# Kernel optimization log

Measured on AMD Instinct MI355X. Metric: run time of the kernel, lower is better.

The kernel has to match this reference:

```python
import jax, jax.numpy as jnp
import numpy as np

N = 20000        # total nodes in batched graph
E = 160000       # edges (avg in-degree 8)
D_IN = 512
D_OUT = 512
MAX_DEG = 10
BN_EPS = 1e-5


def setup_inputs() -> dict:
    key = jax.random.key(0)
    ks = jax.random.split(key, 8)
    feats = jax.random.normal(ks[0], (N, D_IN), dtype=jnp.float32)
    src = jax.random.randint(ks[1], (E,), 0, N)
    dst = jax.random.randint(ks[2], (E,), 0, N)
    # Wl[d], bl[d]: lins_l for degree d (d>=1); Wl[0] is never used since h==0 for deg-0 nodes.
    # Wr[0], bl[0] play the role of lin_zero_deg; Wr[d] (d>=1) are the bias-free lins_r.
    Wl = jax.random.normal(ks[3], (MAX_DEG + 1, D_IN, D_OUT), dtype=jnp.float32) * 0.02
    Wr = jax.random.normal(ks[4], (MAX_DEG + 1, D_IN, D_OUT), dtype=jnp.float32) * 0.02
    bl = jax.random.normal(ks[5], (MAX_DEG + 1, D_OUT), dtype=jnp.float32) * 0.02
    gamma = jnp.ones((D_OUT,), dtype=jnp.float32)
    beta = jnp.zeros((D_OUT,), dtype=jnp.float32)
    return {"feats": feats, "src": src, "dst": dst, "Wl": Wl, "Wr": Wr,
            "bl": bl, "gamma": gamma, "beta": beta}


def reference(feats, src, dst, Wl, Wr, bl, gamma, beta):
    # 1) neighbor sum: h[v] = sum_{(u->v) in E} feats[u]   (fn.copy_u + fn.sum)
    h = jax.ops.segment_sum(feats[src], dst, num_segments=N)  # [N, D_IN]
    # in-degrees, clamped to max_degree
    deg = jnp.clip(jax.ops.segment_sum(jnp.ones((E,), dtype=jnp.int32), dst,
                                       num_segments=N), 0, MAX_DEG)  # [N]
    # 2) degree-bucketed linears, vectorized over the 11 buckets then gathered per node.
    #    out[n] = h[n] @ Wl[deg[n]] + feats[n] @ Wr[deg[n]] + bl[deg[n]]
    #    deg==0 nodes have h==0, so this reduces to lin_zero_deg(feats) = feats@Wr[0]+bl[0].
    Hl = jnp.einsum('ni,dio->dno', h, Wl)      # [11, N, D_OUT]
    Hr = jnp.einsum('ni,dio->dno', feats, Wr)  # [11, N, D_OUT]
    out = (Hl + Hr + bl[:, None, :])[deg, jnp.arange(N)]  # [N, D_OUT]
    # 3) batchnorm (training mode: batch stats, biased variance)
    mean = out.mean(axis=0)
    var = out.var(axis=0)
    out = (out - mean) * jax.lax.rsqrt(var + BN_EPS) * gamma + beta
    # 4) max aggregation over graph with self loops (fn.copy_u + fn.max)
    self_ids = jnp.arange(N)
    src_s = jnp.concatenate([src, self_ids])
    dst_s = jnp.concatenate([dst, self_ids])
    out = jax.ops.segment_max(out[src_s], dst_s, num_segments=N)  # [N, D_OUT]
    return out
```

## Files before the change

kernel.cpp:

```cpp
#include <hip/hip_runtime.h>
#include <hip/hip_bf16.h>
#include <stdint.h>

#define N_NODES 20000
#define N_EDGES 160000
#define DIN 512
#define DOUT 512
#define NBUCKET 11
#define KDIM 1024
#define MAXTILES 90
#define BN_EPS 1e-5f
#define CAP 64
#define CAST_BLOCKS (N_NODES / 4)
#define WT_BLOCKS ((KDIM / 32) * (DOUT / 32) * NBUCKET)
#define BUCKET_BLOCKS ((N_NODES + 255) / 256)

typedef float f32x4 __attribute__((ext_vector_type(4)));
typedef __attribute__((ext_vector_type(8))) __bf16 bf16x8;

static __device__ __forceinline__ unsigned short f2bf(float f) {
    union { float f; unsigned u; } v; v.f = f;
    unsigned r = v.u + 0x7FFFu + ((v.u >> 16) & 1u);
    return (unsigned short)(r >> 16);
}
static __device__ __forceinline__ float bflo(unsigned p) {
    union { unsigned u; float f; } v; v.u = p << 16; return v.f;
}
static __device__ __forceinline__ float bfhi(unsigned p) {
    union { unsigned u; float f; } v; v.u = p & 0xFFFF0000u; return v.f;
}
static __device__ __forceinline__ unsigned packbf(float lo, float hi) {
    return (unsigned)f2bf(lo) | ((unsigned)f2bf(hi) << 16);
}

static __device__ __forceinline__ void gload_lds16(const unsigned short* g, unsigned short* l) {
    __builtin_amdgcn_global_load_lds(
        (const __attribute__((address_space(1))) unsigned int*)g,
        (__attribute__((address_space(3))) unsigned int*)l, 16, 0, 0);
}

__global__ void k_scatter(const int* __restrict__ src, const int* __restrict__ dst,
                          int* __restrict__ cursor, int* __restrict__ eidx2) {
    int e = blockIdx.x * 256 + threadIdx.x;
    if (e >= N_EDGES) return;
    int v = dst[e];
    int slot = atomicAdd(&cursor[v], 1);
    if (slot < CAP) eidx2[v * CAP + slot] = src[e];
}

__global__ __launch_bounds__(256)
void k_prep(const float* __restrict__ feats, const float* __restrict__ Wl,
            const float* __restrict__ Wr, const int* __restrict__ cursor,
            unsigned short* __restrict__ X, unsigned short* __restrict__ Wt,
            int* __restrict__ bucket_cnt, int* __restrict__ bucket_nodes) {
    int b = blockIdx.x;
    int t = threadIdx.x;
    if (b < CAST_BLOCKS) {
        int n = b * 4 + (t >> 6);
        int col = (t & 63) * 8;
        f32x4 a = *(const f32x4*)(feats + (size_t)n * DIN + col);
        f32x4 c = *(const f32x4*)(feats + (size_t)n * DIN + col + 4);
        uint4 p;
        p.x = packbf(a[0], a[1]); p.y = packbf(a[2], a[3]);
        p.z = packbf(c[0], c[1]); p.w = packbf(c[2], c[3]);
        *(uint4*)(X + (size_t)n * KDIM + DIN + col) = p;
        return;
    }
    if (b < CAST_BLOCKS + WT_BLOCKS) {
        __shared__ float tile[32][33];
        int idx = b - CAST_BLOCKS;
        int d = idx / (32 * 16);
        int rem = idx % (32 * 16);
        int k0 = (rem & 31) * 32;
        int n0 = (rem >> 5) * 32;
        int c = t & 31, r0 = t >> 5;
        const float* srcp = (k0 < DIN) ? (Wl + (size_t)d * DIN * DOUT)
                                       : (Wr + (size_t)d * DIN * DOUT - (size_t)DIN * DOUT);
        for (int rr = 0; rr < 4; ++rr) {
            int r = r0 + rr * 8;
            tile[r][c] = srcp[(size_t)(k0 + r) * DOUT + n0 + c];
        }
        __syncthreads();
        for (int rr = 0; rr < 4; ++rr) {
            int r = r0 + rr * 8;
            Wt[((size_t)d * DOUT + n0 + r) * KDIM + k0 + c] = f2bf(tile[c][r]);
        }
        return;
    }
    __shared__ int lhist[NBUCKET];
    __shared__ int lbase[NBUCKET];
    if (t < NBUCKET) lhist[t] = 0;
    __syncthreads();
    int v = (b - CAST_BLOCKS - WT_BLOCKS) * 256 + t;
    int d = -1, slot = 0;
    if (v < N_NODES) {
        d = min(cursor[v], NBUCKET - 1);
        slot = atomicAdd(&lhist[d], 1);
    }
    __syncthreads();
    if (t < NBUCKET && lhist[t] > 0) lbase[t] = atomicAdd(&bucket_cnt[t], lhist[t]);
    __syncthreads();
    if (v < N_NODES) bucket_nodes[d * N_NODES + lbase[d] + slot] = v;
}

__global__ __launch_bounds__(256)
void k_build_x(const int* __restrict__ eidx2, const int* __restrict__ cursor,
               unsigned short* __restrict__ X) {
    int n = blockIdx.x * 4 + (threadIdx.x >> 6);
    int col = (threadIdx.x & 63) * 8;
    const int* adj = eidx2 + (size_t)n * CAP;
    int e = min(cursor[n], CAP);
    float acc[8] = {0,0,0,0,0,0,0,0};
    int i = 0;
    for (; i + 3 < e; i += 4) {
        int u0 = adj[i], u1 = adj[i+1], u2 = adj[i+2], u3 = adj[i+3];
        uint4 p0 = *(const uint4*)(X + (size_t)u0 * KDIM + DIN + col);
        uint4 p1 = *(const uint4*)(X + (size_t)u1 * KDIM + DIN + col);
        uint4 p2 = *(const uint4*)(X + (size_t)u2 * KDIM + DIN + col);
        uint4 p3 = *(const uint4*)(X + (size_t)u3 * KDIM + DIN + col);
        acc[0] += bflo(p0.x) + bflo(p1.x) + bflo(p2.x) + bflo(p3.x);
        acc[1] += bfhi(p0.x) + bfhi(p1.x) + bfhi(p2.x) + bfhi(p3.x);
        acc[2] += bflo(p0.y) + bflo(p1.y) + bflo(p2.y) + bflo(p3.y);
        acc[3] += bfhi(p0.y) + bfhi(p1.y) + bfhi(p2.y) + bfhi(p3.y);
        acc[4] += bflo(p0.z) + bflo(p1.z) + bflo(p2.z) + bflo(p3.z);
        acc[5] += bfhi(p0.z) + bfhi(p1.z) + bfhi(p2.z) + bfhi(p3.z);
        acc[6] += bflo(p0.w) + bflo(p1.w) + bflo(p2.w) + bflo(p3.w);
        acc[7] += bfhi(p0.w) + bfhi(p1.w) + bfhi(p2.w) + bfhi(p3.w);
    }
    for (; i < e; ++i) {
        int u = adj[i];
        uint4 p = *(const uint4*)(X + (size_t)u * KDIM + DIN + col);
        acc[0] += bflo(p.x); acc[1] += bfhi(p.x); acc[2] += bflo(p.y); acc[3] += bfhi(p.y);
        acc[4] += bflo(p.z); acc[5] += bfhi(p.z); acc[6] += bflo(p.w); acc[7] += bfhi(p.w);
    }
    uint4 o;
    o.x = packbf(acc[0], acc[1]); o.y = packbf(acc[2], acc[3]);
    o.z = packbf(acc[4], acc[5]); o.w = packbf(acc[6], acc[7]);
    *(uint4*)(X + (size_t)n * KDIM + col) = o;
}

__global__ __launch_bounds__(512, 2)
void k_gemm(const unsigned short* __restrict__ X, const unsigned short* __restrict__ Wt,
            const int* __restrict__ bucket_nodes, const int* __restrict__ bucket_cnt,
            const float* __restrict__ bl, unsigned short* __restrict__ out_pre,
            float* __restrict__ bn_sum, float* __restrict__ bn_sumsq) {
    int idx = blockIdx.x;
    int d = -1, m0 = 0, accum = 0, cnt = 0;
    for (int b = 0; b < NBUCKET; ++b) {
        int c = bucket_cnt[b];
        int nt = (c + 255) >> 8;
        if (d < 0 && idx < accum + nt) { d = b; m0 = (idx - accum) * 256; cnt = c; }
        accum += nt;
    }
    if (d < 0) return;
    int n0 = blockIdx.y * 256;

    __shared__ __align__(16) unsigned short AkLds[2][2][256 * 32];
    __shared__ __align__(16) unsigned short BkLds[2][2][256 * 32];
    __shared__ int ridS[256];
    __shared__ float colsum[256], colsq[256];

    int t = threadIdx.x;
    if (t < 256) {
        int gm = m0 + t;
        ridS[t] = (gm < cnt) ? bucket_nodes[d * N_NODES + gm] : -1;
        colsum[t] = 0.f; colsq[t] = 0.f;
    }
    __syncthreads();

    int w = t >> 6, l = t & 63;
    int wr = w >> 2, wc = w & 3;
    int lm = l & 15, q = l >> 4;

    int srow = t >> 2;
    int sslot = t & 3;
    int seg = sslot ^ ((srow >> 1) & 3);
    int ridA0 = max(ridS[srow], 0);
    int ridA1 = max(ridS[srow + 128], 0);
    const unsigned short* gA0 = X + (size_t)ridA0 * KDIM + seg * 8;
    const unsigned short* gA1 = X + (size_t)ridA1 * KDIM + seg * 8;
    const unsigned short* gB0 = Wt + ((size_t)d * DOUT + n0 + srow) * KDIM + seg * 8;
    const unsigned short* gB1 = Wt + ((size_t)d * DOUT + n0 + srow + 128) * KDIM + seg * 8;

    int swz = (lm >> 1) & 3;
    int slotrd = ((q ^ swz) & 3) * 8;
    int aoff = (wr * 128 + lm) * 32 + slotrd;
    int boff = (wc * 64 + lm) * 32 + slotrd;

    f32x4 acc[8][4];
#pragma unroll
    for (int i = 0; i < 8; ++i)
#pragma unroll
        for (int j = 0; j < 4; ++j) acc[i][j] = (f32x4){0, 0, 0, 0};

    auto STAGE = [&](int kt, int kh, int bsel) {
        int go = kt * 64 + kh * 32;
        gload_lds16(gA0 + go, &AkLds[bsel][kh][w * 512]);
        gload_lds16(gA1 + go, &AkLds[bsel][kh][4096 + w * 512]);
        gload_lds16(gB0 + go, &BkLds[bsel][kh][w * 512]);
        gload_lds16(gB1 + go, &BkLds[bsel][kh][4096 + w * 512]);
    };
    auto COMPUTE = [&](int bsel, int kh) {
        bf16x8 af[8], bfr[4];
        const unsigned short* Ab = &AkLds[bsel][kh][0];
        const unsigned short* Bb = &BkLds[bsel][kh][0];
#pragma unroll
        for (int mf = 0; mf < 8; ++mf)
            af[mf] = *(const bf16x8*)&Ab[aoff + mf * 512];
#pragma unroll
        for (int nf = 0; nf < 4; ++nf)
            bfr[nf] = *(const bf16x8*)&Bb[boff + nf * 512];
        __builtin_amdgcn_s_setprio(1);
#pragma unroll
        for (int mf = 0; mf < 8; ++mf)
#pragma unroll
            for (int nf = 0; nf < 4; ++nf)
                acc[mf][nf] = __builtin_amdgcn_mfma_f32_16x16x32_bf16(af[mf], bfr[nf], acc[mf][nf], 0, 0, 0);
        __builtin_amdgcn_s_setprio(0);
    };

    STAGE(0, 0, 0);
    STAGE(0, 1, 0);
    STAGE(1, 0, 1);
    asm volatile("s_waitcnt vmcnt(8)" ::: "memory");
    __builtin_amdgcn_s_barrier();
    asm volatile("" ::: "memory");

#pragma unroll 1
    for (int kt = 0; kt < KDIM / 64; ++kt) {
        int buf = kt & 1;
        if (kt < 15) STAGE(kt + 1, 1, buf ^ 1);
        COMPUTE(buf, 0);
        if (kt < 15) asm volatile("s_waitcnt vmcnt(8)" ::: "memory");
        else         asm volatile("s_waitcnt vmcnt(0)" ::: "memory");
        __builtin_amdgcn_s_barrier();
        asm volatile("" ::: "memory");
        if (kt < 14) STAGE(kt + 2, 0, buf);
        COMPUTE(buf, 1);
        if (kt < 14)       asm volatile("s_waitcnt vmcnt(8)" ::: "memory");
        else if (kt == 14) asm volatile("s_waitcnt vmcnt(4)" ::: "memory");
        __builtin_amdgcn_s_barrier();
        asm volatile("" ::: "memory");
    }

    const float* blr = bl + d * DOUT + n0;
    float vsum[4] = {0, 0, 0, 0}, vsq[4] = {0, 0, 0, 0};
#pragma unroll
    for (int mf = 0; mf < 8; ++mf) {
#pragma unroll
        for (int rr = 0; rr < 4; ++rr) {
            int row = wr * 128 + mf * 16 + q * 4 + rr;
            int grow = ridS[row];
            if (grow < 0) continue;
            unsigned short* orow = out_pre + (size_t)grow * DOUT + n0;
#pragma unroll
            for (int nf = 0; nf < 4; ++nf) {
                int col = wc * 64 + nf * 16 + lm;
                float v = acc[mf][nf][rr] + blr[col];
                orow[col] = f2bf(v);
                vsum[nf] += v; vsq[nf] += v * v;
            }
        }
    }
#pragma unroll
    for (int nf = 0; nf < 4; ++nf) {
        vsum[nf] += __shfl_xor(vsum[nf], 16, 64);
        vsum[nf] += __shfl_xor(vsum[nf], 32, 64);
        vsq[nf]  += __shfl_xor(vsq[nf], 16, 64);
        vsq[nf]  += __shfl_xor(vsq[nf], 32, 64);
    }
    if (q == 0) {
#pragma unroll
        for (int nf = 0; nf < 4; ++nf) {
            atomicAdd(&colsum[wc * 64 + nf * 16 + lm], vsum[nf]);
            atomicAdd(&colsq[wc * 64 + nf * 16 + lm], vsq[nf]);
        }
    }
    __syncthreads();
    if (t < 256) {
        atomicAdd(&bn_sum[n0 + t], colsum[t]);
        atomicAdd(&bn_sumsq[n0 + t], colsq[t]);
    }
}

__global__ __launch_bounds__(256)
void k_max(const unsigned short* __restrict__ out_pre, const int* __restrict__ eidx2,
           const int* __restrict__ cursor, const float* __restrict__ bn_sum,
           const float* __restrict__ bn_sumsq, const float* __restrict__ gamma,
           const float* __restrict__ beta, float* __restrict__ out) {
    int n = blockIdx.x * 4 + (threadIdx.x >> 6);
    int col = (threadIdx.x & 63) * 8;
    const int* adj = eidx2 + (size_t)n * CAP;
    int e = min(cursor[n], CAP);
    float mx[8];
    {
        uint4 p = *(const uint4*)(out_pre + (size_t)n * DOUT + col);
        mx[0] = bflo(p.x); mx[1] = bfhi(p.x); mx[2] = bflo(p.y); mx[3] = bfhi(p.y);
        mx[4] = bflo(p.z); mx[5] = bfhi(p.z); mx[6] = bflo(p.w); mx[7] = bfhi(p.w);
    }
    int i = 0;
    for (; i + 3 < e; i += 4) {
        int u0 = adj[i], u1 = adj[i+1], u2 = adj[i+2], u3 = adj[i+3];
        uint4 p0 = *(const uint4*)(out_pre + (size_t)u0 * DOUT + col);
        uint4 p1 = *(const uint4*)(out_pre + (size_t)u1 * DOUT + col);
        uint4 p2 = *(const uint4*)(out_pre + (size_t)u2 * DOUT + col);
        uint4 p3 = *(const uint4*)(out_pre + (size_t)u3 * DOUT + col);
        mx[0] = fmaxf(mx[0], fmaxf(fmaxf(bflo(p0.x), bflo(p1.x)), fmaxf(bflo(p2.x), bflo(p3.x))));
        mx[1] = fmaxf(mx[1], fmaxf(fmaxf(bfhi(p0.x), bfhi(p1.x)), fmaxf(bfhi(p2.x), bfhi(p3.x))));
        mx[2] = fmaxf(mx[2], fmaxf(fmaxf(bflo(p0.y), bflo(p1.y)), fmaxf(bflo(p2.y), bflo(p3.y))));
        mx[3] = fmaxf(mx[3], fmaxf(fmaxf(bfhi(p0.y), bfhi(p1.y)), fmaxf(bfhi(p2.y), bfhi(p3.y))));
        mx[4] = fmaxf(mx[4], fmaxf(fmaxf(bflo(p0.z), bflo(p1.z)), fmaxf(bflo(p2.z), bflo(p3.z))));
        mx[5] = fmaxf(mx[5], fmaxf(fmaxf(bfhi(p0.z), bfhi(p1.z)), fmaxf(bfhi(p2.z), bfhi(p3.z))));
        mx[6] = fmaxf(mx[6], fmaxf(fmaxf(bflo(p0.w), bflo(p1.w)), fmaxf(bflo(p2.w), bflo(p3.w))));
        mx[7] = fmaxf(mx[7], fmaxf(fmaxf(bfhi(p0.w), bfhi(p1.w)), fmaxf(bfhi(p2.w), bfhi(p3.w))));
    }
    for (; i < e; ++i) {
        int u = adj[i];
        uint4 p = *(const uint4*)(out_pre + (size_t)u * DOUT + col);
        mx[0] = fmaxf(mx[0], bflo(p.x)); mx[1] = fmaxf(mx[1], bfhi(p.x));
        mx[2] = fmaxf(mx[2], bflo(p.y)); mx[3] = fmaxf(mx[3], bfhi(p.y));
        mx[4] = fmaxf(mx[4], bflo(p.z)); mx[5] = fmaxf(mx[5], bfhi(p.z));
        mx[6] = fmaxf(mx[6], bflo(p.w)); mx[7] = fmaxf(mx[7], bfhi(p.w));
    }
    const float inv_n = 1.0f / (float)N_NODES;
    f32x4 r0, r1;
#pragma unroll
    for (int jj = 0; jj < 8; ++jj) {
        int c = col + jj;
        float mean = bn_sum[c] * inv_n;
        float var = bn_sumsq[c] * inv_n - mean * mean;
        float sc = gamma[c] * rsqrtf(var + BN_EPS);
        float sh = beta[c] - mean * sc;
        float v = mx[jj] * sc + sh;
        if (jj < 4) r0[jj] = v; else r1[jj - 4] = v;
    }
    *(f32x4*)(out + (size_t)n * DOUT + col) = r0;
    *(f32x4*)(out + (size_t)n * DOUT + col + 4) = r1;
}

extern "C" void kernel_launch(void* const* d_in, const int* in_sizes, int n_in,
                              void* d_out, int out_size, void* d_ws, size_t ws_size,
                              hipStream_t stream) {
    const float* feats = (const float*)d_in[0];
    const int*   src   = (const int*)d_in[1];
    const int*   dst   = (const int*)d_in[2];
    const float* Wl    = (const float*)d_in[3];
    const float* Wr    = (const float*)d_in[4];
    const float* bl    = (const float*)d_in[5];
    const float* gamma = (const float*)d_in[6];
    const float* beta  = (const float*)d_in[7];
    float* out = (float*)d_out;

    char* ws = (char*)d_ws;
    size_t off = 0;
    auto alloc = [&](size_t bytes) -> void* {
        off = (off + 255) & ~(size_t)255;
        void* p = ws + off;
        off += bytes;
        return p;
    };

    int*   cursor     = (int*)alloc(N_NODES * 4);
    int*   bucket_cnt = (int*)alloc(16 * 4);
    float* bn_sum     = (float*)alloc(DOUT * 4);
    float* bn_sumsq   = (float*)alloc(DOUT * 4);
    size_t zbytes = off;

    int* bucket_nodes = (int*)alloc((size_t)NBUCKET * N_NODES * 4);
    int* eidx2        = (int*)alloc((size_t)N_NODES * CAP * 4);
    unsigned short* X  = (unsigned short*)alloc((size_t)N_NODES * KDIM * 2);
    unsigned short* Wt = (unsigned short*)alloc((size_t)NBUCKET * DOUT * KDIM * 2);
    unsigned short* out_pre = (unsigned short*)alloc((size_t)N_NODES * DOUT * 2);

    hipMemsetAsync(d_ws, 0, zbytes, stream);

    k_scatter<<<(N_EDGES + 255) / 256, 256, 0, stream>>>(src, dst, cursor, eidx2);
    k_prep<<<CAST_BLOCKS + WT_BLOCKS + BUCKET_BLOCKS, 256, 0, stream>>>(
        feats, Wl, Wr, cursor, X, Wt, bucket_cnt, bucket_nodes);
    k_build_x<<<N_NODES / 4, 256, 0, stream>>>(eidx2, cursor, X);
    k_gemm<<<dim3(MAXTILES, 2), 512, 0, stream>>>(
        X, Wt, bucket_nodes, bucket_cnt, bl, out_pre, bn_sum, bn_sumsq);
    k_max<<<N_NODES / 4, 256, 0, stream>>>(out_pre, eidx2, cursor, bn_sum, bn_sumsq, gamma, beta, out);
}
```

Baseline: 228.4 us.

## Use 4-slot LDS ring pipeline and 1D grid with tile/column-half block ordering

Replaces the two-buffer, two-half K staging with a four-slot ring that keeps three 32-wide K chunks in flight. This leaves one barrier per chunk and a deeper prefetch. The 2D grid becomes a 1D grid of 192 blocks that interleaves groups of 8 row tiles with both column halves, aiming for better L2 reuse of weights and A rows across co-scheduled blocks. The grid now covers up to 96 tiles instead of 90, so surplus blocks exit early.

```diff
diff --git a/kernel.cpp b/kernel.cpp
--- a/kernel.cpp
+++ b/kernel.cpp
@@ -8,12 +8,12 @@
 #define DOUT 512
 #define NBUCKET 11
 #define KDIM 1024
-#define MAXTILES 90
 #define BN_EPS 1e-5f
 #define CAP 64
 #define CAST_BLOCKS (N_NODES / 4)
 #define WT_BLOCKS ((KDIM / 32) * (DOUT / 32) * NBUCKET)
 #define BUCKET_BLOCKS ((N_NODES + 255) / 256)
+#define GEMM_BLOCKS 192
 
 typedef float f32x4 __attribute__((ext_vector_type(4)));
 typedef __attribute__((ext_vector_type(8))) __bf16 bf16x8;
@@ -144,19 +144,20 @@
             const int* __restrict__ bucket_nodes, const int* __restrict__ bucket_cnt,
             const float* __restrict__ bl, unsigned short* __restrict__ out_pre,
             float* __restrict__ bn_sum, float* __restrict__ bn_sumsq) {
-    int idx = blockIdx.x;
+    int b = blockIdx.x;
+    int tile = (b >> 4) * 8 + (b & 7);
+    int n0 = ((b >> 3) & 1) * 256;
     int d = -1, m0 = 0, accum = 0, cnt = 0;
-    for (int b = 0; b < NBUCKET; ++b) {
-        int c = bucket_cnt[b];
+    for (int bb = 0; bb < NBUCKET; ++bb) {
+        int c = bucket_cnt[bb];
         int nt = (c + 255) >> 8;
-        if (d < 0 && idx < accum + nt) { d = b; m0 = (idx - accum) * 256; cnt = c; }
+        if (d < 0 && tile < accum + nt) { d = bb; m0 = (tile - accum) * 256; cnt = c; }
         accum += nt;
     }
     if (d < 0) return;
-    int n0 = blockIdx.y * 256;
-
-    __shared__ __align__(16) unsigned short AkLds[2][2][256 * 32];
-    __shared__ __align__(16) unsigned short BkLds[2][2][256 * 32];
+
+    __shared__ __align__(16) unsigned short AkLds[4][256 * 32];
+    __shared__ __align__(16) unsigned short BkLds[4][256 * 32];
     __shared__ int ridS[256];
     __shared__ float colsum[256], colsq[256];
 
@@ -193,17 +194,19 @@
 #pragma unroll
         for (int j = 0; j < 4; ++j) acc[i][j] = (f32x4){0, 0, 0, 0};
 
-    auto STAGE = [&](int kt, int kh, int bsel) {
-        int go = kt * 64 + kh * 32;
-        gload_lds16(gA0 + go, &AkLds[bsel][kh][w * 512]);
-        gload_lds16(gA1 + go, &AkLds[bsel][kh][4096 + w * 512]);
-        gload_lds16(gB0 + go, &BkLds[bsel][kh][w * 512]);
-        gload_lds16(gB1 + go, &BkLds[bsel][kh][4096 + w * 512]);
+    auto STAGE = [&](int qq) {
+        int go = qq * 32;
+        int sl = qq & 3;
+        gload_lds16(gA0 + go, &AkLds[sl][w * 512]);
+        gload_lds16(gA1 + go, &AkLds[sl][4096 + w * 512]);
+        gload_lds16(gB0 + go, &BkLds[sl][w * 512]);
+        gload_lds16(gB1 + go, &BkLds[sl][4096 + w * 512]);
     };
-    auto COMPUTE = [&](int bsel, int kh) {
+    auto COMPUTE = [&](int ph) {
+        int sl = ph & 3;
         bf16x8 af[8], bfr[4];
-        const unsigned short* Ab = &AkLds[bsel][kh][0];
-        const unsigned short* Bb = &BkLds[bsel][kh][0];
+        const unsigned short* Ab = &AkLds[sl][0];
+        const unsigned short* Bb = &BkLds[sl][0];
 #pragma unroll
         for (int mf = 0; mf < 8; ++mf)
             af[mf] = *(const bf16x8*)&Ab[aoff + mf * 512];
@@ -219,26 +222,18 @@
         __builtin_amdgcn_s_setprio(0);
     };
 
-    STAGE(0, 0, 0);
-    STAGE(0, 1, 0);
-    STAGE(1, 0, 1);
+    STAGE(0); STAGE(1); STAGE(2);
     asm volatile("s_waitcnt vmcnt(8)" ::: "memory");
     __builtin_amdgcn_s_barrier();
     asm volatile("" ::: "memory");
 
 #pragma unroll 1
-    for (int kt = 0; kt < KDIM / 64; ++kt) {
-        int buf = kt & 1;
-        if (kt < 15) STAGE(kt + 1, 1, buf ^ 1);
-        COMPUTE(buf, 0);
-        if (kt < 15) asm volatile("s_waitcnt vmcnt(8)" ::: "memory");
-        else         asm volatile("s_waitcnt vmcnt(0)" ::: "memory");
-        __builtin_amdgcn_s_barrier();
-        asm volatile("" ::: "memory");
-        if (kt < 14) STAGE(kt + 2, 0, buf);
-        COMPUTE(buf, 1);
-        if (kt < 14)       asm volatile("s_waitcnt vmcnt(8)" ::: "memory");
-        else if (kt == 14) asm volatile("s_waitcnt vmcnt(4)" ::: "memory");
+    for (int p = 0; p < 32; ++p) {
+        if (p < 29) STAGE(p + 3);
+        COMPUTE(p);
+        if (p < 29)       asm volatile("s_waitcnt vmcnt(8)" ::: "memory");
+        else if (p == 29) asm volatile("s_waitcnt vmcnt(4)" ::: "memory");
+        else              asm volatile("s_waitcnt vmcnt(0)" ::: "memory");
         __builtin_amdgcn_s_barrier();
         asm volatile("" ::: "memory");
     }
@@ -378,7 +373,7 @@
     k_prep<<<CAST_BLOCKS + WT_BLOCKS + BUCKET_BLOCKS, 256, 0, stream>>>(
         feats, Wl, Wr, cursor, X, Wt, bucket_cnt, bucket_nodes);
     k_build_x<<<N_NODES / 4, 256, 0, stream>>>(eidx2, cursor, X);
-    k_gemm<<<dim3(MAXTILES, 2), 512, 0, stream>>>(
+    k_gemm<<<dim3(GEMM_BLOCKS), 512, 0, stream>>>(
         X, Wt, bucket_nodes, bucket_cnt, bl, out_pre, bn_sum, bn_sumsq);
     k_max<<<N_NODES / 4, 256, 0, stream>>>(out_pre, eidx2, cursor, bn_sum, bn_sumsq, gamma, beta, out);
 }
```

New measurement: 236.5 us. 1.04x slower.
